# Optimization experiments

Measured on AMD Instinct MI355X. Metric: run time of the kernel, lower is better.

Reference implementation:

```python
import jax, jax.numpy as jnp
import numpy as np

N, D, K = 50000, 512, 32  # n_nodes, dim_in, max neighbors (padded ragged edge_dict)


def setup_inputs() -> dict:
    key = jax.random.key(0)
    k1, k2, k3, k4, k5, k6, k7 = jax.random.split(key, 7)
    feats = jax.random.normal(k1, (N, D), dtype=jnp.float32)
    neighbors = jax.random.randint(k2, (N, K), 0, N)          # padded neighbor ids
    deg = jax.random.randint(k3, (N,), 0, K + 1)               # valid neighbor count (0 == leaf node branch)
    s = 1.0 / np.sqrt(D)  # torch nn.Linear default init range
    wq_w = jax.random.uniform(k4, (D,), jnp.float32, -s, s)
    wq_b = jax.random.uniform(k5, (), jnp.float32, -s, s)
    wk_w = jax.random.uniform(k6, (D,), jnp.float32, -s, s)
    wk_b = jax.random.uniform(k7, (), jnp.float32, -s, s)
    return dict(feats=feats, wq_w=wq_w, wq_b=wq_b, wk_w=wk_w, wk_b=wk_b,
                neighbors=neighbors, deg=deg)


def reference(feats, wq_w, wq_b, wk_w, wk_b, neighbors, deg):
    # Faithful to the original: feats is updated IN PLACE node-by-node, so later
    # nodes read already-updated neighbor features -> sequential lax.scan.
    arange_k = jnp.arange(neighbors.shape[1])
    NEG = jnp.float32(-1e9)

    def step(f, inp):
        i, nbr, d = inp
        mask = (arange_k < d).astype(f.dtype)      # [K] valid-neighbor mask
        nb = f[nbr]                                 # [K, D] neighbor gather
        ei = jnp.dot(f[i], wq_w) + wq_b             # scalar: w_q(center)
        ej = nb @ wk_w + wk_b                       # [K]:    w_k(neighbors)
        eij = ei * ej
        a = jax.nn.softmax(jnp.where(mask > 0, eij, NEG)) * mask  # softmax over dim 0
        upd = a @ nb                                # [D] weighted sum (zero when deg==0)
        new = f[i] + upd                            # in-place add_ on center row
        f = f.at[i].set(new)
        return f, new

    _, rows = jax.lax.scan(step, feats, (jnp.arange(feats.shape[0]), neighbors, deg))
    # Original returns torch.LongTensor(edge_feats) (a lossy int cast of the updated
    # rows); we return the float rows, which carry the actual computed math.
    return rows
```

## Files before the change

kernel.cpp:

```cpp
#include <hip/hip_runtime.h>
#include <hip/hip_fp16.h>


constexpr int NN   = 50000;
constexpr int D    = 512;
constexpr int K    = 32;
constexpr int D4   = D / 4;
constexpr int DU16 = D / 2;

typedef float        v4f __attribute__((ext_vector_type(4)));
typedef unsigned int v4u __attribute__((ext_vector_type(4)));

__device__ __forceinline__ void store_u4_llc(unsigned int* p, v4u v) {
    asm volatile("global_store_dwordx4 %0, %1, off sc0 sc1"
                 :: "v"(p), "v"(v) : "memory");
}
__device__ __forceinline__ void store_f4_llc(float* p, float4 v) {
    v4f vv; vv.x = v.x; vv.y = v.y; vv.z = v.z; vv.w = v.w;
    asm volatile("global_store_dwordx4 %0, %1, off sc0 sc1"
                 :: "v"(p), "v"(vv) : "memory");
}
__device__ __forceinline__ float4 load_f4_nt(const float4* p) {
    v4f r = __builtin_nontemporal_load((const v4f*)p);
    float4 f; f.x = r.x; f.y = r.y; f.z = r.z; f.w = r.w; return f;
}
__device__ __forceinline__ void store_f4_nt(float4* p, float4 v) {
    v4f vv; vv.x = v.x; vv.y = v.y; vv.z = v.z; vv.w = v.w;
    __builtin_nontemporal_store(vv, (v4f*)p);
}
__device__ __forceinline__ unsigned int packh2(float a, float b) {
    __half2 h = __floats2half2_rn(a, b);
    return *reinterpret_cast<unsigned int*>(&h);
}
__device__ __forceinline__ float2 unpackh2(unsigned int u) {
    __half2 h = *reinterpret_cast<__half2*>(&u);
    return __half22float2(h);
}

__global__ __launch_bounds__(256) void precomp_kernel(
    const float* __restrict__ feats,
    const float* __restrict__ wq_w, const float* __restrict__ wq_b,
    const float* __restrict__ wk_w, const float* __restrict__ wk_b,
    float* __restrict__ ei, float* __restrict__ ej_orig,
    unsigned int* __restrict__ feats16)
{
    int gw   = (int)((blockIdx.x * blockDim.x + threadIdx.x) >> 6);
    int lane = threadIdx.x & 63;
    if (gw >= NN) return;
    const float4* row = (const float4*)feats + (size_t)gw * D4;
    const float4* q4  = (const float4*)wq_w;
    const float4* k4  = (const float4*)wk_w;
    float4 v0 = load_f4_nt(row + 2 * lane), v1 = load_f4_nt(row + 2 * lane + 1);
    float4 q0 = q4[2 * lane],  q1 = q4[2 * lane + 1];
    float4 k0 = k4[2 * lane],  k1 = k4[2 * lane + 1];
    float dq = v0.x*q0.x + v0.y*q0.y + v0.z*q0.z + v0.w*q0.w
             + v1.x*q1.x + v1.y*q1.y + v1.z*q1.z + v1.w*q1.w;
    float dk = v0.x*k0.x + v0.y*k0.y + v0.z*k0.z + v0.w*k0.w
             + v1.x*k1.x + v1.y*k1.y + v1.z*k1.z + v1.w*k1.w;
#pragma unroll
    for (int off = 32; off > 0; off >>= 1) {
        dq += __shfl_down(dq, off, 64);
        dk += __shfl_down(dk, off, 64);
    }
    if (feats16) {
        v4u p;
        p.x = packh2(v0.x, v0.y); p.y = packh2(v0.z, v0.w);
        p.z = packh2(v1.x, v1.y); p.w = packh2(v1.z, v1.w);
        *(v4u*)(feats16 + (size_t)gw * DU16 + 4 * lane) = p;
    }
    if (lane == 0) {
        ei[gw]      = dq + wq_b[0];
        ej_orig[gw] = dk + wk_b[0];
    }
}

__global__ __launch_bounds__(256, 4) void attn_dataflow_h16(
    const float* __restrict__ feats,
    const int* __restrict__ neighbors, const int* __restrict__ deg,
    const float* __restrict__ ei_arr, const float* __restrict__ ej_orig,
    const float* __restrict__ wk_b,
    const unsigned int* __restrict__ feats16, unsigned int* __restrict__ out16,
    int* ej_new, float* out)
{
    const int lane   = threadIdx.x & 63;
    const int gwave  = (int)((blockIdx.x * blockDim.x + threadIdx.x) >> 6);
    const int nwaves = (int)((gridDim.x * blockDim.x) >> 6);
    const float4* f4  = (const float4*)feats;
    const float   wkb = wk_b[0];

    for (int id = gwave; id < NN; id += nwaves) {
        const int d = deg[id];
        int nbr = 0;
        if (lane < K) nbr = neighbors[(size_t)id * K + lane];
        const bool valid = lane < d;
        const bool isdep = valid && (nbr < id);

        const float4 c0 = load_f4_nt(f4 + (size_t)id * D4 + 2 * lane);
        const float4 c1 = load_f4_nt(f4 + (size_t)id * D4 + 2 * lane + 1);
        const float eii  = ei_arr[id];
        const float ejoc = ej_orig[id];

        float ejraw = 0.f, eij = 0.f;
        if (valid && !isdep) { ejraw = ej_orig[nbr]; eij = eii * ejraw; }

        float4 acc0 = {0.f, 0.f, 0.f, 0.f};
        float4 acc1 = {0.f, 0.f, 0.f, 0.f};
        float m = -3.0e38f, s = 0.f, se = 0.f;

        unsigned long long pend = __ballot(valid && !isdep);
        unsigned long long wait = __ballot(isdep);

        while (pend | wait) {
            if (!pend) {
                int pv = 0;
                const bool w = (wait >> lane) & 1ULL;
                if (w) pv = __hip_atomic_load(&ej_new[nbr], __ATOMIC_RELAXED,
                                              __HIP_MEMORY_SCOPE_AGENT);
                unsigned long long ready = __ballot(w && pv != 0);
                if (!ready) { __builtin_amdgcn_s_sleep(1); continue; }
                if (w && pv != 0) { ejraw = __int_as_float(pv); eij = eii * ejraw; }
                pend = ready;
                wait &= ~ready;
            }
            int js_[8]; float ee[8], ev2[8]; int klast = 0;
#pragma unroll
            for (int t = 0; t < 8; ++t) {
                const bool has = (pend != 0);
                int k = has ? ((int)__ffsll(pend) - 1) : klast;
                if (has) pend &= pend - 1;
                klast = k;
                float ev = __shfl(eij, k, 64);
                ee[t]  = has ? ev : -3.0e38f;
                ev2[t] = __shfl(ejraw, k, 64);
                js_[t] = __shfl(nbr, k, 64);
            }
            v4u pv8[8];
#pragma unroll
            for (int t = 0; t < 8; ++t) {
                const unsigned int* sp = ((js_[t] < id) ? out16 : feats16)
                                         + (size_t)js_[t] * DU16 + 4 * lane;
                pv8[t] = *(const v4u*)sp;
            }
            float mb = m;
#pragma unroll
            for (int t = 0; t < 8; ++t) mb = fmaxf(mb, ee[t]);
            if (mb > m) {
                const float r = __expf(m - mb);
                acc0.x *= r; acc0.y *= r; acc0.z *= r; acc0.w *= r;
                acc1.x *= r; acc1.y *= r; acc1.z *= r; acc1.w *= r;
                s *= r; se *= r; m = mb;
            }
#pragma unroll
            for (int t = 0; t < 8; ++t) {
                const float wt = __expf(ee[t] - m);
                s  += wt;
                se += wt * ev2[t];
                float2 f0 = unpackh2(pv8[t].x), f1 = unpackh2(pv8[t].y);
                float2 f2 = unpackh2(pv8[t].z), f3 = unpackh2(pv8[t].w);
                acc0.x += wt * f0.x; acc0.y += wt * f0.y;
                acc0.z += wt * f1.x; acc0.w += wt * f1.y;
                acc1.x += wt * f2.x; acc1.y += wt * f2.y;
                acc1.z += wt * f3.x; acc1.w += wt * f3.y;
            }
        }

        const float inv_s = (s > 0.f) ? (1.0f / s) : 0.f;
        float4 g0 = {c0.x + acc0.x * inv_s, c0.y + acc0.y * inv_s,
                     c0.z + acc0.z * inv_s, c0.w + acc0.w * inv_s};
        float4 g1 = {c1.x + acc1.x * inv_s, c1.y + acc1.y * inv_s,
                     c1.z + acc1.z * inv_s, c1.w + acc1.w * inv_s};

        v4u pg;
        pg.x = packh2(g0.x, g0.y); pg.y = packh2(g0.z, g0.w);
        pg.z = packh2(g1.x, g1.y); pg.w = packh2(g1.z, g1.w);
        store_u4_llc(out16 + (size_t)id * DU16 + 4 * lane, pg);

        const float ejn = ejoc + ((s > 0.f) ? (se * inv_s - wkb) : 0.f);
        int bits = __float_as_int(ejn);
        if (bits == 0) bits = 1;

        __builtin_amdgcn_s_waitcnt(0);
        if (lane == 0)
            __hip_atomic_store(&ej_new[id], bits,
                               __ATOMIC_RELAXED, __HIP_MEMORY_SCOPE_AGENT);

        float4* orow4 = (float4*)out + (size_t)id * D4;
        store_f4_nt(orow4 + 2 * lane,     g0);
        store_f4_nt(orow4 + 2 * lane + 1, g1);
    }
}

__global__ __launch_bounds__(256, 4) void attn_dataflow_f32(
    const float* __restrict__ feats,
    const int* __restrict__ neighbors, const int* __restrict__ deg,
    const float* __restrict__ ei_arr, const float* __restrict__ ej_orig,
    const float* __restrict__ wk_w, const float* __restrict__ wk_b,
    int* ej_new, float* out)
{
    const int lane   = threadIdx.x & 63;
    const int gwave  = (int)((blockIdx.x * blockDim.x + threadIdx.x) >> 6);
    const int nwaves = (int)((gridDim.x * blockDim.x) >> 6);
    const float4* f4  = (const float4*)feats;
    const float4* o4r = (const float4*)out;
    const float4* wk4 = (const float4*)wk_w;
    const float   wkb = wk_b[0];

    for (int id = gwave; id < NN; id += nwaves) {
        const int d = deg[id];
        int nbr = 0;
        if (lane < K) nbr = neighbors[(size_t)id * K + lane];
        const bool valid = lane < d;
        const bool isdep = valid && (nbr < id);

        const float4 c0 = f4[(size_t)id * D4 + lane];
        const float4 c1 = f4[(size_t)id * D4 + lane + 64];
        const float eii = ei_arr[id];

        float eij = 0.f;
        if (valid && !isdep) eij = eii * ej_orig[nbr];

        float4 acc0 = {0.f, 0.f, 0.f, 0.f};
        float4 acc1 = {0.f, 0.f, 0.f, 0.f};
        float m = -3.0e38f, s = 0.f;

        unsigned long long pend = __ballot(valid && !isdep);
        unsigned long long wait = __ballot(isdep);

        while (pend | wait) {
            if (!pend) {
                int pv = 0;
                const bool w = (wait >> lane) & 1ULL;
                if (w) pv = __hip_atomic_load(&ej_new[nbr], __ATOMIC_RELAXED,
                                              __HIP_MEMORY_SCOPE_AGENT);
                unsigned long long ready = __ballot(w && pv != 0);
                if (!ready) { __builtin_amdgcn_s_sleep(1); continue; }
                if (w && pv != 0) eij = eii * __int_as_float(pv);
                pend = ready;
                wait &= ~ready;
            }
            int cnt = 0;
            int   js[4]; float ee[4];
#pragma unroll
            for (int t = 0; t < 4; ++t) {
                if (pend) {
                    int k = (int)__ffsll(pend) - 1;
                    pend &= pend - 1;
                    ee[cnt] = __shfl(eij, k, 64);
                    js[cnt] = __shfl(nbr, k, 64);
                    ++cnt;
                }
            }
            float4 v0[4], v1[4];
#pragma unroll
            for (int t = 0; t < 4; ++t) {
                if (t < cnt) {
                    const float4* sp = (js[t] < id) ? (o4r + (size_t)js[t] * D4)
                                                    : (f4  + (size_t)js[t] * D4);
                    v0[t] = sp[lane];
                    v1[t] = sp[lane + 64];
                }
            }
            float mb = m;
#pragma unroll
            for (int t = 0; t < 4; ++t) if (t < cnt) mb = fmaxf(mb, ee[t]);
            if (mb > m) {
                const float r = __expf(m - mb);
                acc0.x *= r; acc0.y *= r; acc0.z *= r; acc0.w *= r;
                acc1.x *= r; acc1.y *= r; acc1.z *= r; acc1.w *= r;
                s *= r; m = mb;
            }
#pragma unroll
            for (int t = 0; t < 4; ++t) {
                if (t < cnt) {
                    const float wt = __expf(ee[t] - m);
                    s += wt;
                    acc0.x += wt * v0[t].x; acc0.y += wt * v0[t].y;
                    acc0.z += wt * v0[t].z; acc0.w += wt * v0[t].w;
                    acc1.x += wt * v1[t].x; acc1.y += wt * v1[t].y;
                    acc1.z += wt * v1[t].z; acc1.w += wt * v1[t].w;
                }
            }
        }

        const float inv_s = (s > 0.f) ? (1.0f / s) : 0.f;
        float4 g0 = {c0.x + acc0.x * inv_s, c0.y + acc0.y * inv_s,
                     c0.z + acc0.z * inv_s, c0.w + acc0.w * inv_s};
        float4 g1 = {c1.x + acc1.x * inv_s, c1.y + acc1.y * inv_s,
                     c1.z + acc1.z * inv_s, c1.w + acc1.w * inv_s};
        float* orow = out + (size_t)id * D;
        store_f4_llc(orow + 4 * lane,        g0);
        store_f4_llc(orow + 4 * (lane + 64), g1);

        float4 w0 = wk4[lane], w1 = wk4[lane + 64];
        float pd = g0.x * w0.x + g0.y * w0.y + g0.z * w0.z + g0.w * w0.w
                 + g1.x * w1.x + g1.y * w1.y + g1.z * w1.z + g1.w * w1.w;
#pragma unroll
        for (int off = 32; off > 0; off >>= 1)
            pd += __shfl_xor(pd, off, 64);

        int bits = __float_as_int(pd + wkb);
        if (bits == 0) bits = 1;

        __builtin_amdgcn_s_waitcnt(0);
        if (lane == 0)
            __hip_atomic_store(&ej_new[id], bits,
                               __ATOMIC_RELAXED, __HIP_MEMORY_SCOPE_AGENT);
    }
}

extern "C" void kernel_launch(void* const* d_in, const int* in_sizes, int n_in,
                              void* d_out, int out_size, void* d_ws, size_t ws_size,
                              hipStream_t stream)
{
    const float* feats     = (const float*)d_in[0];
    const float* wq_w      = (const float*)d_in[1];
    const float* wq_b      = (const float*)d_in[2];
    const float* wk_w      = (const float*)d_in[3];
    const float* wk_b      = (const float*)d_in[4];
    const int*   neighbors = (const int*)d_in[5];
    const int*   deg       = (const int*)d_in[6];
    float*       out       = (float*)d_out;

    char*  ws      = (char*)d_ws;
    int*   ej_new  = (int*)ws;
    float* ei      = (float*)(ej_new + NN + 64);
    float* ej_orig = ei + NN;
    size_t scal_end = (size_t)((char*)(ej_orig + NN) - ws);
    size_t f16_off  = (scal_end + 1023) & ~(size_t)1023;
    size_t f16_need = 2ull * NN * DU16 * sizeof(unsigned int);
    const bool use16 = (ws_size >= f16_off + f16_need);
    unsigned int* feats16 = (unsigned int*)(ws + f16_off);
    unsigned int* out16   = feats16 + (size_t)NN * DU16;

    (void)hipMemsetAsync(d_ws, 0, (size_t)NN * sizeof(int), stream);

    dim3 pb(256), pg((NN + 3) / 4);
    precomp_kernel<<<pg, pb, 0, stream>>>(feats, wq_w, wq_b, wk_w, wk_b,
                                          ei, ej_orig, use16 ? feats16 : nullptr);

    if (use16) {
        attn_dataflow_h16<<<dim3(1024), dim3(256), 0, stream>>>(
            feats, neighbors, deg, ei, ej_orig, wk_b,
            feats16, out16, ej_new, out);
    } else {
        attn_dataflow_f32<<<dim3(1024), dim3(256), 0, stream>>>(
            feats, neighbors, deg, ei, ej_orig, wk_w, wk_b, ej_new, out);
    }
}
```

Baseline: 374.8 us.

## Split scalar ej dependency from row readiness to publish ej early

Each node now waits only for its dependent neighbors' scalar ej values, computes the full softmax weights with wave reductions, and publishes its own ej_new before the row accumulation. A separate row_flag array signals when the fp16 output row is written, and dependents wait on that flag before gathering the row. This shortens the critical path of the scalar dependency chain so later nodes can compute their weights sooner, and it removes the online-softmax rescaling. The cost is a second flag array, an extra memset, and two rounds of polling per node. Nontemporal loads and stores are also replaced with ordinary ones.

```diff
diff --git a/kernel.cpp b/kernel.cpp
--- a/kernel.cpp
+++ b/kernel.cpp
@@ -19,14 +19,6 @@
     v4f vv; vv.x = v.x; vv.y = v.y; vv.z = v.z; vv.w = v.w;
     asm volatile("global_store_dwordx4 %0, %1, off sc0 sc1"
                  :: "v"(p), "v"(vv) : "memory");
-}
-__device__ __forceinline__ float4 load_f4_nt(const float4* p) {
-    v4f r = __builtin_nontemporal_load((const v4f*)p);
-    float4 f; f.x = r.x; f.y = r.y; f.z = r.z; f.w = r.w; return f;
-}
-__device__ __forceinline__ void store_f4_nt(float4* p, float4 v) {
-    v4f vv; vv.x = v.x; vv.y = v.y; vv.z = v.z; vv.w = v.w;
-    __builtin_nontemporal_store(vv, (v4f*)p);
 }
 __device__ __forceinline__ unsigned int packh2(float a, float b) {
     __half2 h = __floats2half2_rn(a, b);
@@ -50,7 +42,7 @@
     const float4* row = (const float4*)feats + (size_t)gw * D4;
     const float4* q4  = (const float4*)wq_w;
     const float4* k4  = (const float4*)wk_w;
-    float4 v0 = load_f4_nt(row + 2 * lane), v1 = load_f4_nt(row + 2 * lane + 1);
+    float4 v0 = row[2 * lane], v1 = row[2 * lane + 1];
     float4 q0 = q4[2 * lane],  q1 = q4[2 * lane + 1];
     float4 k0 = k4[2 * lane],  k1 = k4[2 * lane + 1];
     float dq = v0.x*q0.x + v0.y*q0.y + v0.z*q0.z + v0.w*q0.w
@@ -80,7 +72,7 @@
     const float* __restrict__ ei_arr, const float* __restrict__ ej_orig,
     const float* __restrict__ wk_b,
     const unsigned int* __restrict__ feats16, unsigned int* __restrict__ out16,
-    int* ej_new, float* out)
+    int* ej_new, int* row_flag, float* out)
 {
     const int lane   = threadIdx.x & 63;
     const int gwave  = (int)((blockIdx.x * blockDim.x + threadIdx.x) >> 6);
@@ -95,43 +87,72 @@
         const bool valid = lane < d;
         const bool isdep = valid && (nbr < id);
 
-        const float4 c0 = load_f4_nt(f4 + (size_t)id * D4 + 2 * lane);
-        const float4 c1 = load_f4_nt(f4 + (size_t)id * D4 + 2 * lane + 1);
+        const float4 c0 = f4[(size_t)id * D4 + 2 * lane];
+        const float4 c1 = f4[(size_t)id * D4 + 2 * lane + 1];
         const float eii  = ei_arr[id];
         const float ejoc = ej_orig[id];
 
-        float ejraw = 0.f, eij = 0.f;
+        float ejraw = 0.f, eij = -3.0e38f;
         if (valid && !isdep) { ejraw = ej_orig[nbr]; eij = eii * ejraw; }
+
+        unsigned long long wait = __ballot(isdep);
+        while (wait) {
+            int pv = 0;
+            const bool w = (wait >> lane) & 1ULL;
+            if (w) pv = __hip_atomic_load(&ej_new[nbr], __ATOMIC_RELAXED,
+                                          __HIP_MEMORY_SCOPE_AGENT);
+            unsigned long long ready = __ballot(w && pv != 0);
+            if (w && pv != 0) { ejraw = __int_as_float(pv); eij = eii * ejraw; }
+            wait &= ~ready;
+            if (wait && !ready) __builtin_amdgcn_s_sleep(1);
+        }
+        float m = eij;
+#pragma unroll
+        for (int off = 32; off > 0; off >>= 1)
+            m = fmaxf(m, __shfl_xor(m, off, 64));
+        const float wt = valid ? __expf(eij - m) : 0.f;
+        float s = wt, se = wt * ejraw;
+#pragma unroll
+        for (int off = 32; off > 0; off >>= 1) {
+            s  += __shfl_xor(s,  off, 64);
+            se += __shfl_xor(se, off, 64);
+        }
+        const float inv_s = (s > 0.f) ? (1.0f / s) : 0.f;
+
+        {
+            const float ejn = ejoc + ((s > 0.f) ? (se * inv_s - wkb) : 0.f);
+            int bits = __float_as_int(ejn);
+            if (bits == 0) bits = 1;
+            if (lane == 0)
+                __hip_atomic_store(&ej_new[id], bits,
+                                   __ATOMIC_RELAXED, __HIP_MEMORY_SCOPE_AGENT);
+        }
 
         float4 acc0 = {0.f, 0.f, 0.f, 0.f};
         float4 acc1 = {0.f, 0.f, 0.f, 0.f};
-        float m = -3.0e38f, s = 0.f, se = 0.f;
-
-        unsigned long long pend = __ballot(valid && !isdep);
-        unsigned long long wait = __ballot(isdep);
-
-        while (pend | wait) {
+        unsigned long long pend  = __ballot(valid && !isdep);
+        unsigned long long wait2 = __ballot(isdep);
+
+        while (pend | wait2) {
             if (!pend) {
-                int pv = 0;
-                const bool w = (wait >> lane) & 1ULL;
-                if (w) pv = __hip_atomic_load(&ej_new[nbr], __ATOMIC_RELAXED,
+                int rv = 0;
+                const bool w = (wait2 >> lane) & 1ULL;
+                if (w) rv = __hip_atomic_load(&row_flag[nbr], __ATOMIC_RELAXED,
                                               __HIP_MEMORY_SCOPE_AGENT);
-                unsigned long long ready = __ballot(w && pv != 0);
+                unsigned long long ready = __ballot(w && rv != 0);
                 if (!ready) { __builtin_amdgcn_s_sleep(1); continue; }
-                if (w && pv != 0) { ejraw = __int_as_float(pv); eij = eii * ejraw; }
                 pend = ready;
-                wait &= ~ready;
-            }
-            int js_[8]; float ee[8], ev2[8]; int klast = 0;
+                wait2 &= ~ready;
+            }
+            int js_[8]; float ww[8]; int klast = 0;
 #pragma unroll
             for (int t = 0; t < 8; ++t) {
                 const bool has = (pend != 0);
                 int k = has ? ((int)__ffsll(pend) - 1) : klast;
                 if (has) pend &= pend - 1;
                 klast = k;
-                float ev = __shfl(eij, k, 64);
-                ee[t]  = has ? ev : -3.0e38f;
-                ev2[t] = __shfl(ejraw, k, 64);
+                float w8 = __shfl(wt, k, 64);
+                ww[t]  = has ? w8 : 0.f;
                 js_[t] = __shfl(nbr, k, 64);
             }
             v4u pv8[8];
@@ -141,30 +162,18 @@
                                          + (size_t)js_[t] * DU16 + 4 * lane;
                 pv8[t] = *(const v4u*)sp;
             }
-            float mb = m;
-#pragma unroll
-            for (int t = 0; t < 8; ++t) mb = fmaxf(mb, ee[t]);
-            if (mb > m) {
-                const float r = __expf(m - mb);
-                acc0.x *= r; acc0.y *= r; acc0.z *= r; acc0.w *= r;
-                acc1.x *= r; acc1.y *= r; acc1.z *= r; acc1.w *= r;
-                s *= r; se *= r; m = mb;
-            }
 #pragma unroll
             for (int t = 0; t < 8; ++t) {
-                const float wt = __expf(ee[t] - m);
-                s  += wt;
-                se += wt * ev2[t];
+                const float a = ww[t];
                 float2 f0 = unpackh2(pv8[t].x), f1 = unpackh2(pv8[t].y);
                 float2 f2 = unpackh2(pv8[t].z), f3 = unpackh2(pv8[t].w);
-                acc0.x += wt * f0.x; acc0.y += wt * f0.y;
-                acc0.z += wt * f1.x; acc0.w += wt * f1.y;
-                acc1.x += wt * f2.x; acc1.y += wt * f2.y;
-                acc1.z += wt * f3.x; acc1.w += wt * f3.y;
-            }
-        }
-
-        const float inv_s = (s > 0.f) ? (1.0f / s) : 0.f;
+                acc0.x += a * f0.x; acc0.y += a * f0.y;
+                acc0.z += a * f1.x; acc0.w += a * f1.y;
+                acc1.x += a * f2.x; acc1.y += a * f2.y;
+                acc1.z += a * f3.x; acc1.w += a * f3.y;
+            }
+        }
+
         float4 g0 = {c0.x + acc0.x * inv_s, c0.y + acc0.y * inv_s,
                      c0.z + acc0.z * inv_s, c0.w + acc0.w * inv_s};
         float4 g1 = {c1.x + acc1.x * inv_s, c1.y + acc1.y * inv_s,
@@ -175,18 +184,14 @@
         pg.z = packh2(g1.x, g1.y); pg.w = packh2(g1.z, g1.w);
         store_u4_llc(out16 + (size_t)id * DU16 + 4 * lane, pg);
 
-        const float ejn = ejoc + ((s > 0.f) ? (se * inv_s - wkb) : 0.f);
-        int bits = __float_as_int(ejn);
-        if (bits == 0) bits = 1;
-
         __builtin_amdgcn_s_waitcnt(0);
         if (lane == 0)
-            __hip_atomic_store(&ej_new[id], bits,
+            __hip_atomic_store(&row_flag[id], 1,
                                __ATOMIC_RELAXED, __HIP_MEMORY_SCOPE_AGENT);
 
         float4* orow4 = (float4*)out + (size_t)id * D4;
-        store_f4_nt(orow4 + 2 * lane,     g0);
-        store_f4_nt(orow4 + 2 * lane + 1, g1);
+        orow4[2 * lane]     = g0;
+        orow4[2 * lane + 1] = g1;
     }
 }
 
@@ -321,10 +326,11 @@
     const int*   deg       = (const int*)d_in[6];
     float*       out       = (float*)d_out;
 
-    char*  ws      = (char*)d_ws;
-    int*   ej_new  = (int*)ws;
-    float* ei      = (float*)(ej_new + NN + 64);
-    float* ej_orig = ei + NN;
+    char*  ws       = (char*)d_ws;
+    int*   ej_new   = (int*)ws;
+    int*   row_flag = ej_new + NN + 64;
+    float* ei       = (float*)(row_flag + NN + 64);
+    float* ej_orig  = ei + NN;
     size_t scal_end = (size_t)((char*)(ej_orig + NN) - ws);
     size_t f16_off  = (scal_end + 1023) & ~(size_t)1023;
     size_t f16_need = 2ull * NN * DU16 * sizeof(unsigned int);
@@ -332,7 +338,7 @@
     unsigned int* feats16 = (unsigned int*)(ws + f16_off);
     unsigned int* out16   = feats16 + (size_t)NN * DU16;
 
-    (void)hipMemsetAsync(d_ws, 0, (size_t)NN * sizeof(int), stream);
+    (void)hipMemsetAsync(d_ws, 0, (size_t)(2 * NN + 128) * sizeof(int), stream);
 
     dim3 pb(256), pg((NN + 3) / 4);
     precomp_kernel<<<pg, pb, 0, stream>>>(feats, wq_w, wq_b, wk_w, wk_b,
@@ -341,7 +347,7 @@
     if (use16) {
         attn_dataflow_h16<<<dim3(1024), dim3(256), 0, stream>>>(
             feats, neighbors, deg, ei, ej_orig, wk_b,
-            feats16, out16, ej_new, out);
+            feats16, out16, ej_new, row_flag, out);
     } else {
         attn_dataflow_f32<<<dim3(1024), dim3(256), 0, stream>>>(
             feats, neighbors, deg, ei, ej_orig, wk_w, wk_b, ej_new, out);
```

Result: no change. 372.3 us (-0.7%).
